# Kernel tuning notes

Hardware: AMD Instinct MI355X
Metric: run time of the kernel (lower is better)

The kernel has to match this reference:

```python
import jax, jax.numpy as jnp
import numpy as np

N_PROT = 100000
N_DRUG = 20000
D = 128
E_PPI = 1600000
E_DTI = 800000
LN_EPS = 1e-5


def setup_inputs() -> dict:
    key = jax.random.key(0)
    ks = jax.random.split(key, 11)
    s = 1.0 / np.sqrt(D)
    return {
        "x_prot": jax.random.normal(ks[0], (N_PROT, D), jnp.float32),
        "x_drug": jax.random.normal(ks[1], (N_DRUG, D), jnp.float32),
        "W_gcn": jax.random.normal(ks[2], (D, D), jnp.float32) * s,
        "b_gcn": jnp.zeros((D,), jnp.float32),
        "W_td": jax.random.normal(ks[3], (D, D), jnp.float32) * s,
        "b_td": jnp.zeros((D,), jnp.float32),
        "W_pr": jax.random.normal(ks[4], (D, D), jnp.float32) * s,
        "b_pr": jnp.zeros((D,), jnp.float32),
        "ppi_edge_index": jax.random.randint(ks[5], (2, E_PPI), 0, N_PROT),
        "dti_drug": jax.random.randint(ks[6], (E_DTI,), 0, N_DRUG),
        "dti_prot": jax.random.randint(ks[7], (E_DTI,), 0, N_PROT),
    }


def _gcn_conv(x, W, b, edge_index, num_nodes):
    # PyG GCNConv: add self-loops, symmetric D^-1/2 (A+I) D^-1/2 normalization.
    xw = x @ W  # [N, D_out]
    loops = jnp.arange(num_nodes)
    row = jnp.concatenate([edge_index[0], loops])
    col = jnp.concatenate([edge_index[1], loops])
    deg = jax.ops.segment_sum(jnp.ones_like(col, dtype=xw.dtype), col,
                              num_segments=num_nodes)
    dinv = jnp.where(deg > 0, jax.lax.rsqrt(deg), 0.0)
    norm = dinv[row] * dinv[col]  # [E+N]
    msg = xw[row] * norm[:, None]
    return jax.ops.segment_sum(msg, col, num_segments=num_nodes) + b


def _scatter_mean(vals, idx, num_segments):
    s = jax.ops.segment_sum(vals, idx, num_segments=num_segments)
    cnt = jax.ops.segment_sum(jnp.ones_like(idx, dtype=vals.dtype), idx,
                              num_segments=num_segments)
    return s / jnp.maximum(cnt, 1.0)[:, None]


def _layer_norm(y):
    mu = jnp.mean(y, axis=-1, keepdims=True)
    var = jnp.mean(jnp.square(y - mu), axis=-1, keepdims=True)
    return (y - mu) * jax.lax.rsqrt(var + LN_EPS)


def reference(x_prot, x_drug, W_gcn, b_gcn, W_td, b_td, W_pr, b_pr,
              ppi_edge_index, dti_drug, dti_prot):
    # 'protein' branch of rela_graph_node_update.forward
    x1 = _gcn_conv(x_prot, W_gcn, b_gcn, ppi_edge_index, N_PROT)
    msgs = (x_drug @ W_td + b_td)[dti_drug]  # gather drug messages per dti edge
    x2 = _scatter_mean(msgs, dti_prot, N_PROT)
    x3 = x_prot @ W_pr + b_pr
    return _layer_norm(x1 + x2 + x3 + 1e-6)
```

## Files before the change

kernel.cpp:

```cpp
#include <hip/hip_runtime.h>
#include <hip/hip_bf16.h>

#define D 128
#define NPBK 256
#define NBMAX 512
#define TILE_A 4096
#define SEGMAX 8192

typedef unsigned int uint;
typedef unsigned short ushort;
typedef __attribute__((ext_vector_type(8))) short short8;
typedef __attribute__((ext_vector_type(4))) float f32x4;
typedef __attribute__((ext_vector_type(2))) float f32x2;
typedef __attribute__((ext_vector_type(2))) uint u32x2;

static __device__ __forceinline__ float2 bf16x2(uint u) {
  float2 r;
  r.x = __uint_as_float(u << 16);
  r.y = __uint_as_float(u & 0xffff0000u);
  return r;
}

static __device__ __forceinline__ f32x2 bf16x2v(uint u) {
  u32x2 t = {u << 16, u & 0xffff0000u};
  return __builtin_bit_cast(f32x2, t);
}

static __device__ __forceinline__ uint pack_bf16x2(float a, float b) {
  __hip_bfloat162 o;
  o.x = __float2bfloat16(a);
  o.y = __float2bfloat16(b);
  return *reinterpret_cast<uint*>(&o);
}

static __device__ __forceinline__ ushort f2bf(float f) {
  __hip_bfloat16 h = __float2bfloat16(f);
  return *reinterpret_cast<ushort*>(&h);
}
static __device__ __forceinline__ float bf2f(ushort u) {
  return __uint_as_float(((uint)u) << 16);
}

static __device__ __forceinline__ void facc8(f32x2* acc4, uint4 v, f32x2 s2) {
  acc4[0] += s2 * bf16x2v(v.x);
  acc4[1] += s2 * bf16x2v(v.y);
  acc4[2] += s2 * bf16x2v(v.z);
  acc4[3] += s2 * bf16x2v(v.w);
}

__global__ void detect_kernel(const uint* __restrict__ x, int n_words,
                              int* __restrict__ flag) {
  __shared__ float smax[256];
  float m = 0.f;
  for (int i = threadIdx.x; i < n_words; i += 256) {
    float2 v = bf16x2(x[i]);
    float a = fabsf(v.x), b = fabsf(v.y);
    if (!(a <= 1e30f)) a = 1e30f;
    if (!(b <= 1e30f)) b = 1e30f;
    m = fmaxf(m, fmaxf(a, b));
  }
  smax[threadIdx.x] = m;
  __syncthreads();
  for (int s = 128; s > 0; s >>= 1) {
    if (threadIdx.x < s)
      smax[threadIdx.x] = fmaxf(smax[threadIdx.x], smax[threadIdx.x + s]);
    __syncthreads();
  }
  if (threadIdx.x == 0) *flag = (smax[0] > 1e6f) ? 1 : 0;
}

__global__ __launch_bounds__(256) void bucket_hist_kernel(
    const int* __restrict__ ppi_col, const int* __restrict__ dti_prot,
    int* __restrict__ gbh, const uint* __restrict__ xdet,
    int* __restrict__ flag, int e_ppi, int e_dti, int n_prot, int nbk) {
  __shared__ int hist[NBMAX];
  __shared__ float smax[256];
  const int tid = threadIdx.x;

  if (blockIdx.x == 0) {
    float m = 0.f;
    for (int i = tid; i < 4096; i += 256) {
      float2 v = bf16x2(xdet[i]);
      float a = fabsf(v.x), b = fabsf(v.y);
      if (!(a <= 1e30f)) a = 1e30f;
      if (!(b <= 1e30f)) b = 1e30f;
      m = fmaxf(m, fmaxf(a, b));
    }
    smax[tid] = m;
    __syncthreads();
    for (int s = 128; s > 0; s >>= 1) {
      if (tid < s) smax[tid] = fmaxf(smax[tid], smax[tid + s]);
      __syncthreads();
    }
    if (tid == 0) *flag = (smax[0] > 1e6f) ? 1 : 0;
  }

  for (int b = tid; b < nbk; b += 256) hist[b] = 0;
  __syncthreads();
  const int e_tot = e_ppi + e_dti;
  const int base = blockIdx.x * 8192;
#pragma unroll 4
  for (int j = 0; j < 32; ++j) {
    int i = base + j * 256 + tid;
    if (i < e_tot) {
      int dst = (i < e_ppi) ? ppi_col[i] : dti_prot[i - e_ppi];
      if ((unsigned)dst < (unsigned)n_prot) atomicAdd(&hist[dst >> 8], 1);
    }
  }
  __syncthreads();
  for (int b = tid; b < nbk; b += 256) {
    int h = hist[b];
    if (h) atomicAdd(&gbh[b], h);
  }
}

__global__ __launch_bounds__(256) void partition_kernel(
    const int* __restrict__ ppi_row, const int* __restrict__ ppi_col,
    const int* __restrict__ dti_drug, const int* __restrict__ dti_prot,
    const int* __restrict__ gbh, int* __restrict__ gcur, uint* __restrict__ P,
    int e_ppi, int e_dti, int n_prot, int nb) {
  __shared__ int hist[NBMAX];
  __shared__ int sh[NBMAX];
  __shared__ int lbase[NBMAX];
  __shared__ int gbase[NBMAX];
  __shared__ int cur[NBMAX];
  __shared__ int totS;
  __shared__ uint entL[TILE_A];
  __shared__ ushort bktL[TILE_A];
  const int tid = threadIdx.x;
  const int t2 = tid + 256;
  const int base = blockIdx.x * TILE_A;
  const int e_tot = e_ppi + e_dti;

  hist[tid] = 0;
  hist[t2] = 0;
  __syncthreads();

  uint sv[16];
  int dv[16];
#pragma unroll
  for (int j = 0; j < 16; ++j) {
    int i = base + j * 256 + tid;
    int d = -1;
    uint s = 0;
    if (i < e_tot) {
      int src, dst, type;
      if (i < e_ppi) {
        src = ppi_row[i];
        dst = ppi_col[i];
        type = 0;
      } else {
        int k = i - e_ppi;
        src = dti_drug[k];
        dst = dti_prot[k];
        type = 1;
      }
      if ((unsigned)dst < (unsigned)n_prot) {
        d = dst;
        s = (uint)src | ((uint)type << 17);
        atomicAdd(&hist[dst >> 8], 1);
      }
    }
    sv[j] = s;
    dv[j] = d;
  }
  __syncthreads();

  sh[tid] = hist[tid];
  sh[t2] = hist[t2];
  __syncthreads();
  for (int ofs = 1; ofs < NBMAX; ofs <<= 1) {
    int a0 = (tid >= ofs) ? sh[tid - ofs] : 0;
    int a1 = (t2 >= ofs) ? sh[t2 - ofs] : 0;
    __syncthreads();
    sh[tid] += a0;
    sh[t2] += a1;
    __syncthreads();
  }
  for (int b = tid; b < NBMAX; b += 256) {
    int lb = sh[b] - hist[b];
    lbase[b] = lb;
    cur[b] = lb;
  }
  if (tid == 0) totS = sh[NBMAX - 1];
  __syncthreads();

  sh[tid] = (tid < nb) ? gbh[tid] : 0;
  sh[t2] = (t2 < nb) ? gbh[t2] : 0;
  __syncthreads();
  for (int ofs = 1; ofs < NBMAX; ofs <<= 1) {
    int a0 = (tid >= ofs) ? sh[tid - ofs] : 0;
    int a1 = (t2 >= ofs) ? sh[t2 - ofs] : 0;
    __syncthreads();
    sh[tid] += a0;
    sh[t2] += a1;
    __syncthreads();
  }
  for (int b = tid; b < NBMAX; b += 256) {
    int h = hist[b];
    gbase[b] = h ? ((b ? sh[b - 1] : 0) + atomicAdd(&gcur[b], h)) : 0;
  }
  __syncthreads();

#pragma unroll
  for (int j = 0; j < 16; ++j) {
    if (dv[j] >= 0) {
      int b = dv[j] >> 8;
      int r = atomicAdd(&cur[b], 1);
      entL[r] = sv[j] | ((uint)(dv[j] & (NPBK - 1)) << 18);
      bktL[r] = (ushort)b;
    }
  }
  __syncthreads();

  const int tot = totS;
  for (int u = tid; u < tot; u += 256) {
    int b = bktL[u];
    P[gbase[b] + (u - lbase[b])] = entL[u];
  }
}

__global__ __launch_bounds__(1024) void place_count_kernel(
    const uint* __restrict__ P, const int* __restrict__ gbh,
    uint* __restrict__ csr, int* __restrict__ deg, float* __restrict__ dinv,
    float* __restrict__ invcnt, int* __restrict__ offsets, int n_prot,
    int nbk) {
  __shared__ int degL[NPBK], cntL[NPBK];
  __shared__ int cp[NPBK], cd[NPBK];
  __shared__ int sc[NPBK];
  __shared__ int gsh[NBMAX];
  __shared__ int startS, endS;
  __shared__ uint srt[SEGMAX];
  const int tid = threadIdx.x;
  const int b = blockIdx.x;
  const int node0 = b * NPBK;
  const int nn = min(NPBK, n_prot - node0);

  if (tid < NBMAX) gsh[tid] = (tid < nbk) ? gbh[tid] : 0;
  __syncthreads();
  for (int ofs = 1; ofs < NBMAX; ofs <<= 1) {
    int t = 0;
    if (tid < NBMAX && tid >= ofs) t = gsh[tid - ofs];
    __syncthreads();
    if (tid < NBMAX) gsh[tid] += t;
    __syncthreads();
  }
  if (tid == 0) {
    startS = b ? gsh[b - 1] : 0;
    endS = gsh[b];
  }
  if (tid < NPBK) {
    degL[tid] = 0;
    cntL[tid] = 0;
  }
  __syncthreads();
  const int start = startS, end = endS;
  const int nseg = end - start;

  for (int i = start + tid; i < end; i += 1024) {
    uint p = P[i];
    int nl = (int)(p >> 18);
    if ((p >> 17) & 1u)
      atomicAdd(&cntL[nl], 1);
    else
      atomicAdd(&degL[nl], 1);
  }
  __syncthreads();

  int v = 0;
  if (tid < NPBK) {
    v = (tid < nn) ? (degL[tid] + cntL[tid]) : 0;
    sc[tid] = v;
  }
  __syncthreads();
  for (int ofs = 1; ofs < NPBK; ofs <<= 1) {
    int t = 0;
    if (tid < NPBK && tid >= ofs) t = sc[tid - ofs];
    __syncthreads();
    if (tid < NPBK) sc[tid] += t;
    __syncthreads();
  }
  if (tid < nn) {
    int d = degL[tid], c = cntL[tid];
    int lexcl = sc[tid] - v;
    int node = node0 + tid;
    offsets[node] = start + lexcl;
    deg[node] = d;
    dinv[node] = rsqrtf((float)(d + 1));
    invcnt[node] = 1.0f / fmaxf((float)c, 1.0f);
    cp[tid] = lexcl;
    cd[tid] = lexcl + d;
  }
  if (b == nbk - 1 && tid == 0) offsets[n_prot] = end;
  __syncthreads();

  if (nseg <= SEGMAX) {
    for (int i = start + tid; i < end; i += 1024) {
      uint p = P[i];
      int nl = (int)(p >> 18);
      int pos =
          ((p >> 17) & 1u) ? atomicAdd(&cd[nl], 1) : atomicAdd(&cp[nl], 1);
      srt[pos] = p & 0x1ffffu;
    }
    __syncthreads();
    for (int u = tid; u < nseg; u += 1024) csr[start + u] = srt[u];
  } else {
    for (int i = start + tid; i < end; i += 1024) {
      uint p = P[i];
      int nl = (int)(p >> 18);
      int pos =
          ((p >> 17) & 1u) ? atomicAdd(&cd[nl], 1) : atomicAdd(&cp[nl], 1);
      csr[start + pos] = p & 0x1ffffu;
    }
  }
}

__global__ void count_kernel(const int* __restrict__ ppi_col,
                             const int* __restrict__ dti_prot,
                             int* __restrict__ deg, int* __restrict__ cnt,
                             int e_ppi, int e_dti, int n_prot) {
  int i = blockIdx.x * blockDim.x + threadIdx.x;
  if (i < e_ppi) {
    int c = ppi_col[i];
    if ((unsigned)c < (unsigned)n_prot) atomicAdd(&deg[c], 1);
  } else if (i < e_ppi + e_dti) {
    int c = dti_prot[i - e_ppi];
    if ((unsigned)c < (unsigned)n_prot) atomicAdd(&cnt[c], 1);
  }
}

__global__ void block_sum_kernel(const int* __restrict__ deg,
                                 const int* __restrict__ cnt, int n,
                                 float* __restrict__ dinv,
                                 float* __restrict__ invcnt,
                                 int* __restrict__ bsum) {
  __shared__ int sh[256];
  int i = blockIdx.x * 256 + threadIdx.x;
  int t = 0;
  if (i < n) {
    int d = deg[i], c = cnt[i];
    dinv[i] = rsqrtf((float)(d + 1));
    invcnt[i] = 1.0f / fmaxf((float)c, 1.0f);
    t = d + c;
  }
  sh[threadIdx.x] = t;
  __syncthreads();
  for (int s = 128; s > 0; s >>= 1) {
    if (threadIdx.x < s) sh[threadIdx.x] += sh[threadIdx.x + s];
    __syncthreads();
  }
  if (threadIdx.x == 0) bsum[blockIdx.x] = sh[0];
}

__global__ void scan_bsums_kernel(int* __restrict__ bsum, int nb) {
  __shared__ int sh[1024];
  __shared__ int carry;
  int tid = threadIdx.x;
  if (tid == 0) carry = 0;
  __syncthreads();
  for (int base = 0; base < nb; base += 1024) {
    int i = base + tid;
    int v = (i < nb) ? bsum[i] : 0;
    sh[tid] = v;
    __syncthreads();
    for (int ofs = 1; ofs < 1024; ofs <<= 1) {
      int t = (tid >= ofs) ? sh[tid - ofs] : 0;
      __syncthreads();
      sh[tid] += t;
      __syncthreads();
    }
    if (i < nb) bsum[i] = carry + sh[tid] - v;
    int total = sh[1023];
    __syncthreads();
    if (tid == 0) carry += total;
    __syncthreads();
  }
}

__global__ void scan_final_kernel(const int* __restrict__ deg,
                                  const int* __restrict__ cnt,
                                  const int* __restrict__ bbase,
                                  int* __restrict__ offsets, int n) {
  __shared__ int sh[256];
  int tid = threadIdx.x;
  int i = blockIdx.x * 256 + tid;
  int v = (i < n) ? deg[i] + cnt[i] : 0;
  sh[tid] = v;
  __syncthreads();
  for (int ofs = 1; ofs < 256; ofs <<= 1) {
    int t = (tid >= ofs) ? sh[tid - ofs] : 0;
    __syncthreads();
    sh[tid] += t;
    __syncthreads();
  }
  if (i < n) {
    int excl = bbase[blockIdx.x] + sh[tid] - v;
    offsets[i] = excl;
    if (i == n - 1) offsets[n] = excl + v;
  }
}

__global__ void fill_kernel(const int* __restrict__ ppi_row,
                            const int* __restrict__ ppi_col,
                            const int* __restrict__ dti_drug,
                            const int* __restrict__ dti_prot,
                            const int* __restrict__ offsets,
                            const int* __restrict__ deg,
                            int* __restrict__ fposp, int* __restrict__ fposd,
                            uint* __restrict__ csr, int e_ppi, int e_dti,
                            int n_prot) {
  int i = blockIdx.x * blockDim.x + threadIdx.x;
  if (i < e_ppi) {
    int dst = ppi_col[i];
    if ((unsigned)dst >= (unsigned)n_prot) return;
    int pos = offsets[dst] + atomicAdd(&fposp[dst], 1);
    csr[pos] = (uint)ppi_row[i];
  } else if (i < e_ppi + e_dti) {
    int j = i - e_ppi;
    int dst = dti_prot[j];
    if ((unsigned)dst >= (unsigned)n_prot) return;
    int pos = offsets[dst] + deg[dst] + atomicAdd(&fposd[dst], 1);
    csr[pos] = (uint)dti_drug[j];
  }
}

static __device__ void gemm_prot_body(
    uint4 (*aF)[4][2][64], ushort (*xwl)[128], const void* __restrict__ X,
    const void* __restrict__ Wg, const void* __restrict__ Wp,
    const void* __restrict__ bg, const void* __restrict__ bp,
    const float* __restrict__ dinv, uint* __restrict__ xw2,
    void* __restrict__ outx3, int isf, int M, int bid, int nblk) {
  const int tid = threadIdx.x;
  const int wv = tid >> 6, lane = tid & 63;
  const int cl = lane & 15, kg = lane >> 4;
  const int c = wv * 16 + cl;

  short8 bG[4], bP[4];
#pragma unroll
  for (int kt = 0; kt < 4; ++kt) {
    int k0 = kt * 32 + 8 * kg;
    short8 fg, fp;
    if (isf) {
      const float* WgF = (const float*)Wg;
      const float* WpF = (const float*)Wp;
#pragma unroll
      for (int j = 0; j < 8; ++j) {
        fg[j] = (short)f2bf(WgF[(k0 + j) * D + c]);
        fp[j] = (short)f2bf(WpF[(k0 + j) * D + c]);
      }
    } else {
      const ushort* WgH = (const ushort*)Wg;
      const ushort* WpH = (const ushort*)Wp;
#pragma unroll
      for (int j = 0; j < 8; ++j) {
        fg[j] = (short)WgH[(k0 + j) * D + c];
        fp[j] = (short)WpH[(k0 + j) * D + c];
      }
    }
    bG[kt] = fg;
    bP[kt] = fp;
  }
  float btc;
  {
    float a = isf ? ((const float*)bg)[c] : bf2f(((const ushort*)bg)[c]);
    float b = isf ? ((const float*)bp)[c] : bf2f(((const ushort*)bp)[c]);
    btc = a + b + 1e-6f;
  }

  for (int row0 = bid * 64; row0 < M; row0 += nblk * 64) {
    for (int u = tid; u < 1024; u += 512) {
      int row = u >> 4, kc = u & 15;
      int grow = row0 + row;
      uint4 hi = make_uint4(0, 0, 0, 0), lo = make_uint4(0, 0, 0, 0);
      if (isf) {
        if (grow < M) {
          const float4* Xf = (const float4*)X;
          float4 v0 = Xf[(size_t)grow * 32 + kc * 2];
          float4 v1 = Xf[(size_t)grow * 32 + kc * 2 + 1];
          float v[8] = {v0.x, v0.y, v0.z, v0.w, v1.x, v1.y, v1.z, v1.w};
          uint hw[4], lw[4];
#pragma unroll
          for (int j = 0; j < 4; ++j) {
            ushort h0 = f2bf(v[2 * j]), h1 = f2bf(v[2 * j + 1]);
            ushort l0 = f2bf(v[2 * j] - bf2f(h0));
            ushort l1 = f2bf(v[2 * j + 1] - bf2f(h1));
            hw[j] = (uint)h0 | ((uint)h1 << 16);
            lw[j] = (uint)l0 | ((uint)l1 << 16);
          }
          hi = make_uint4(hw[0], hw[1], hw[2], hw[3]);
          lo = make_uint4(lw[0], lw[1], lw[2], lw[3]);
        }
      } else {
        if (grow < M) hi = ((const uint4*)X)[(size_t)grow * 16 + kc];
      }
      int ln = (kc & 3) * 16 + (row & 15);
      int g = row >> 4, kt = kc >> 2;
      aF[g][kt][0][ln] = hi;
      if (isf) aF[g][kt][1][ln] = lo;
    }
    __syncthreads();

#pragma unroll
    for (int g = 0; g < 4; ++g) {
      f32x4 accG = {0.f, 0.f, 0.f, 0.f};
      f32x4 accP = {0.f, 0.f, 0.f, 0.f};
      uint4 aH[4];
#pragma unroll
      for (int kt = 0; kt < 4; ++kt) aH[kt] = aF[g][kt][0][lane];
#pragma unroll
      for (int kt = 0; kt < 4; ++kt) {
        short8 a = __builtin_bit_cast(short8, aH[kt]);
        accG = __builtin_amdgcn_mfma_f32_16x16x32_bf16(a, bG[kt], accG, 0, 0, 0);
        accP = __builtin_amdgcn_mfma_f32_16x16x32_bf16(a, bP[kt], accP, 0, 0, 0);
      }
      if (isf) {
        uint4 aL[4];
#pragma unroll
        for (int kt = 0; kt < 4; ++kt) aL[kt] = aF[g][kt][1][lane];
#pragma unroll
        for (int kt = 0; kt < 4; ++kt) {
          short8 a = __builtin_bit_cast(short8, aL[kt]);
          accG = __builtin_amdgcn_mfma_f32_16x16x32_bf16(a, bG[kt], accG, 0, 0, 0);
          accP = __builtin_amdgcn_mfma_f32_16x16x32_bf16(a, bP[kt], accP, 0, 0, 0);
        }
      }
      int rl0 = g * 16 + kg * 4;
#pragma unroll
      for (int r = 0; r < 4; ++r) {
        int row = row0 + rl0 + r;
        if (row < M) {
          float dn = dinv[row];
          float gv = accG[r], pv = accP[r];
          xwl[rl0 + r][c] = f2bf(gv * dn);
          float ov = fmaf(gv, dn * dn, pv + btc);
          if (isf)
            ((float*)outx3)[(size_t)row * D + c] = ov;
          else
            ((ushort*)outx3)[(size_t)row * D + c] = f2bf(ov);
        }
      }
    }
    __syncthreads();

    int valid = min(64, M - row0);
    const uint4* src = (const uint4*)xwl;
    uint4* dst = (uint4*)xw2 + (size_t)row0 * 16;
    for (int u = tid; u < valid * 16; u += 512) dst[u] = src[u];
  }
}

static __device__ void gemm_drug_body(uint4 (*aF)[4][2][64], ushort (*yl)[128],
                                      const void* __restrict__ X,
                                      const void* __restrict__ W,
                                      const void* __restrict__ bias,
                                      uint* __restrict__ Y2, int isf, int M,
                                      int bid, int nblk) {
  const int tid = threadIdx.x;
  const int wv = tid >> 6, lane = tid & 63;
  const int cl = lane & 15, kg = lane >> 4;
  const int c = wv * 16 + cl;

  short8 bT[4];
#pragma unroll
  for (int kt = 0; kt < 4; ++kt) {
    int k0 = kt * 32 + 8 * kg;
    short8 ft;
    if (isf) {
      const float* Wf = (const float*)W;
#pragma unroll
      for (int j = 0; j < 8; ++j) ft[j] = (short)f2bf(Wf[(k0 + j) * D + c]);
    } else {
      const ushort* Wh = (const ushort*)W;
#pragma unroll
      for (int j = 0; j < 8; ++j) ft[j] = (short)Wh[(k0 + j) * D + c];
    }
    bT[kt] = ft;
  }
  float btc = isf ? ((const float*)bias)[c] : bf2f(((const ushort*)bias)[c]);

  for (int row0 = bid * 64; row0 < M; row0 += nblk * 64) {
    for (int u = tid; u < 1024; u += 512) {
      int row = u >> 4, kc = u & 15;
      int grow = row0 + row;
      uint4 hi = make_uint4(0, 0, 0, 0), lo = make_uint4(0, 0, 0, 0);
      if (isf) {
        if (grow < M) {
          const float4* Xf = (const float4*)X;
          float4 v0 = Xf[(size_t)grow * 32 + kc * 2];
          float4 v1 = Xf[(size_t)grow * 32 + kc * 2 + 1];
          float v[8] = {v0.x, v0.y, v0.z, v0.w, v1.x, v1.y, v1.z, v1.w};
          uint hw[4], lw[4];
#pragma unroll
          for (int j = 0; j < 4; ++j) {
            ushort h0 = f2bf(v[2 * j]), h1 = f2bf(v[2 * j + 1]);
            ushort l0 = f2bf(v[2 * j] - bf2f(h0));
            ushort l1 = f2bf(v[2 * j + 1] - bf2f(h1));
            hw[j] = (uint)h0 | ((uint)h1 << 16);
            lw[j] = (uint)l0 | ((uint)l1 << 16);
          }
          hi = make_uint4(hw[0], hw[1], hw[2], hw[3]);
          lo = make_uint4(lw[0], lw[1], lw[2], lw[3]);
        }
      } else {
        if (grow < M) hi = ((const uint4*)X)[(size_t)grow * 16 + kc];
      }
      int ln = (kc & 3) * 16 + (row & 15);
      int g = row >> 4, kt = kc >> 2;
      aF[g][kt][0][ln] = hi;
      if (isf) aF[g][kt][1][ln] = lo;
    }
    __syncthreads();

#pragma unroll
    for (int g = 0; g < 4; ++g) {
      f32x4 acc = {0.f, 0.f, 0.f, 0.f};
      uint4 aH[4];
#pragma unroll
      for (int kt = 0; kt < 4; ++kt) aH[kt] = aF[g][kt][0][lane];
#pragma unroll
      for (int kt = 0; kt < 4; ++kt) {
        short8 a = __builtin_bit_cast(short8, aH[kt]);
        acc = __builtin_amdgcn_mfma_f32_16x16x32_bf16(a, bT[kt], acc, 0, 0, 0);
      }
      if (isf) {
        uint4 aL[4];
#pragma unroll
        for (int kt = 0; kt < 4; ++kt) aL[kt] = aF[g][kt][1][lane];
#pragma unroll
        for (int kt = 0; kt < 4; ++kt) {
          short8 a = __builtin_bit_cast(short8, aL[kt]);
          acc = __builtin_amdgcn_mfma_f32_16x16x32_bf16(a, bT[kt], acc, 0, 0, 0);
        }
      }
      int rl0 = g * 16 + kg * 4;
#pragma unroll
      for (int r = 0; r < 4; ++r) {
        int row = row0 + rl0 + r;
        if (row < M) yl[rl0 + r][c] = f2bf(acc[r] + btc);
      }
    }
    __syncthreads();

    int valid = min(64, M - row0);
    const uint4* src = (const uint4*)yl;
    uint4* dst = (uint4*)Y2 + (size_t)row0 * 16;
    for (int u = tid; u < valid * 16; u += 512) dst[u] = src[u];
  }
}

__global__ __launch_bounds__(512) void gemm_fused_kernel(
    const void* __restrict__ Xp, const void* __restrict__ Wg,
    const void* __restrict__ Wp, const void* __restrict__ bg,
    const void* __restrict__ bp, const float* __restrict__ dinv,
    uint* __restrict__ xw2, void* __restrict__ outx3, int Mp, int gp,
    const void* __restrict__ Xd, const void* __restrict__ Wt,
    const void* __restrict__ bt, uint* __restrict__ yd2, int Md,
    const int* __restrict__ flag) {
  __shared__ uint4 aF[4][4][2][64];
  __shared__ ushort tb[64][128];
  const int isf = *flag;
  if ((int)blockIdx.x < gp)
    gemm_prot_body(aF, tb, Xp, Wg, Wp, bg, bp, dinv, xw2, outx3, isf, Mp,
                   blockIdx.x, gp);
  else
    gemm_drug_body(aF, tb, Xd, Wt, bt, yd2, isf, Md, blockIdx.x - gp,
                   gridDim.x - gp);
}

__global__ __launch_bounds__(256) void gather_ln_kernel(
    const uint* __restrict__ xw2, const uint* __restrict__ yd2,
    const float* __restrict__ dinv, const float* __restrict__ invcnt,
    const int* __restrict__ offsets, const int* __restrict__ deg,
    const uint* __restrict__ csr, void* __restrict__ out,
    const int* __restrict__ flag, int node0, int ncount) {
  const int isf = *flag;
  const int nloc = (blockIdx.x * 256 + threadIdx.x) >> 6;
  const int lane = threadIdx.x & 63;
  const int grp = lane >> 4;
  const int li = lane & 15;
  if (nloc >= ncount) return;
  const int node = node0 + nloc;
  const int s0 = offsets[node];
  const int s1 = offsets[node + 1];
  const int sm = s0 + deg[node];
  const float dn = dinv[node], ic = invcnt[node];

  float x3l[8];
  if (isf) {
    const float4* xr = (const float4*)out + (size_t)node * 32 + li * 2;
    float4 x0 = xr[0], x1 = xr[1];
    x3l[0] = x0.x; x3l[1] = x0.y; x3l[2] = x0.z; x3l[3] = x0.w;
    x3l[4] = x1.x; x3l[5] = x1.y; x3l[6] = x1.z; x3l[7] = x1.w;
  } else {
    uint4 xr = ((const uint4*)out)[(size_t)node * 16 + li];
    float2 t0 = bf16x2(xr.x), t1 = bf16x2(xr.y);
    float2 t2 = bf16x2(xr.z), t3 = bf16x2(xr.w);
    x3l[0] = t0.x; x3l[1] = t0.y; x3l[2] = t1.x; x3l[3] = t1.y;
    x3l[4] = t2.x; x3l[5] = t2.y; x3l[6] = t3.x; x3l[7] = t3.y;
  }

  f32x2 acc4[4] = {{0.f, 0.f}, {0.f, 0.f}, {0.f, 0.f}, {0.f, 0.f}};
  const uint4* X4 = (const uint4*)xw2;
  const uint4* Y4 = (const uint4*)yd2;

  for (int base = s0; base < s1;) {
    int m = min(64, s1 - base);
    uint ent = (lane < m) ? csr[base + lane] : 0u;
    int nq = m >> 2;
    int t = 0;
    for (; t + 4 <= nq; t += 4) {
      uint4 w[4];
      f32x2 sc[4];
#pragma unroll
      for (int q = 0; q < 4; ++q) {
        int slot = (t + q) * 4 + grp;
        uint e = __shfl(ent, slot);
        bool isP = (base + slot) < sm;
        const uint4* T = isP ? X4 : Y4;
        w[q] = T[(size_t)e * 16 + li];
        float s = isP ? dn : ic;
        sc[q] = (f32x2){s, s};
      }
#pragma unroll
      for (int q = 0; q < 4; ++q) facc8(acc4, w[q], sc[q]);
    }
    for (; t + 2 <= nq; t += 2) {
      uint4 w0, w1;
      f32x2 sc0, sc1;
      {
        int slot = t * 4 + grp;
        uint e = __shfl(ent, slot);
        bool isP = (base + slot) < sm;
        const uint4* T = isP ? X4 : Y4;
        w0 = T[(size_t)e * 16 + li];
        float s = isP ? dn : ic;
        sc0 = (f32x2){s, s};
      }
      {
        int slot = (t + 1) * 4 + grp;
        uint e = __shfl(ent, slot);
        bool isP = (base + slot) < sm;
        const uint4* T = isP ? X4 : Y4;
        w1 = T[(size_t)e * 16 + li];
        float s = isP ? dn : ic;
        sc1 = (f32x2){s, s};
      }
      facc8(acc4, w0, sc0);
      facc8(acc4, w1, sc1);
    }
    for (; t < nq; ++t) {
      int slot = t * 4 + grp;
      uint e = __shfl(ent, slot);
      bool isP = (base + slot) < sm;
      const uint4* T = isP ? X4 : Y4;
      uint4 wv = T[(size_t)e * 16 + li];
      float s = isP ? dn : ic;
      facc8(acc4, wv, (f32x2){s, s});
    }
    int rem = m & 3;
    if (rem) {
      int slot = nq * 4 + grp;
      uint e = __shfl(ent, slot);
      if (grp < rem) {
        bool isP = (base + slot) < sm;
        const uint4* T = isP ? X4 : Y4;
        uint4 wv = T[(size_t)e * 16 + li];
        float s = isP ? dn : ic;
        facc8(acc4, wv, (f32x2){s, s});
      }
    }
    base += m;
  }

  float v[8];
#pragma unroll
  for (int i = 0; i < 8; ++i) {
    float t = (i & 1) ? acc4[i >> 1].y : acc4[i >> 1].x;
    t += __shfl_xor(t, 16);
    t += __shfl_xor(t, 32);
    v[i] = t + x3l[i];
  }

  float s = 0.f, ss = 0.f;
#pragma unroll
  for (int i = 0; i < 8; ++i) {
    s += v[i];
    ss = fmaf(v[i], v[i], ss);
  }
#pragma unroll
  for (int off = 1; off < 16; off <<= 1) {
    s += __shfl_xor(s, off);
    ss += __shfl_xor(ss, off);
  }
  float mu = s * (1.0f / 128.0f);
  float var = ss * (1.0f / 128.0f) - mu * mu;
  float rs = rsqrtf(var + 1e-5f);
#pragma unroll
  for (int i = 0; i < 8; ++i) v[i] = (v[i] - mu) * rs;

  if (isf) {
    if (grp < 2) {
      float4 o = (grp == 0) ? make_float4(v[0], v[1], v[2], v[3])
                            : make_float4(v[4], v[5], v[6], v[7]);
      ((float4*)out)[(size_t)node * 32 + li * 2 + grp] = o;
    }
  } else {
    if (grp == 0) {
      uint4 o;
      o.x = pack_bf16x2(v[0], v[1]);
      o.y = pack_bf16x2(v[2], v[3]);
      o.z = pack_bf16x2(v[4], v[5]);
      o.w = pack_bf16x2(v[6], v[7]);
      ((uint4*)out)[(size_t)node * 16 + li] = o;
    }
  }
}

extern "C" void kernel_launch(void* const* d_in, const int* in_sizes, int n_in,
                              void* d_out, int out_size, void* d_ws,
                              size_t ws_size, hipStream_t stream) {
  const void* x_prot = d_in[0];
  const void* x_drug = d_in[1];
  const void* W_gcn = d_in[2];
  const void* b_gcn = d_in[3];
  const void* W_td = d_in[4];
  const void* b_td = d_in[5];
  const void* W_pr = d_in[6];
  const void* b_pr = d_in[7];
  const int* ppi = (const int*)d_in[8];
  const int* dti_drug = (const int*)d_in[9];
  const int* dti_prot = (const int*)d_in[10];

  int n_prot = in_sizes[0] / D;
  int n_drug = in_sizes[1] / D;
  int e_ppi = in_sizes[8] / 2;
  int e_dti = in_sizes[9];
  int e_tot = e_ppi + e_dti;
  int nb = (n_prot + 255) / 256;
  int nbk = (n_prot + NPBK - 1) / NPBK;

  char* ws = (char*)d_ws;
  size_t off = 0;
  auto alloc = [&](size_t bytes) {
    void* p = ws + off;
    off = (off + bytes + 255) & ~(size_t)255;
    return p;
  };
  int* flag = (int*)alloc(256);
  uint* xw2 = (uint*)alloc((size_t)n_prot * 64 * 4);
  uint* yd2 = (uint*)alloc((size_t)n_drug * 64 * 4);
  int* deg = (int*)alloc((size_t)n_prot * 4);
  int* cnt = (int*)alloc((size_t)n_prot * 4);
  float* dinv = (float*)alloc((size_t)n_prot * 4);
  float* invcnt = (float*)alloc((size_t)n_prot * 4);
  int* offsets = (int*)alloc((size_t)(n_prot + 1) * 4);
  int* fposp = (int*)alloc((size_t)n_prot * 4);
  int* fposd = (int*)alloc((size_t)n_prot * 4);
  int* bsum = (int*)alloc((size_t)nb * 4);
  int* gbh = (int*)alloc((size_t)NBMAX * 4);
  int* gcur = (int*)alloc((size_t)NBMAX * 4);
  uint* csr = (uint*)alloc((size_t)e_tot * 4);

  if (off > ws_size) return;

  uint* P = xw2;
  bool fast_fill = (n_prot <= (1 << 17)) && (n_drug <= (1 << 17)) &&
                   (nbk <= NBMAX) && ((size_t)e_tot * 4 <= (size_t)n_prot * 256);

  if (fast_fill) {
    hipMemsetAsync(gbh, 0, (size_t)2 * NBMAX * 4, stream);
    bucket_hist_kernel<<<(e_tot + 8191) / 8192, 256, 0, stream>>>(
        ppi + e_ppi, dti_prot, gbh, (const uint*)x_prot, flag, e_ppi, e_dti,
        n_prot, nbk);
    partition_kernel<<<(e_tot + TILE_A - 1) / TILE_A, 256, 0, stream>>>(
        ppi, ppi + e_ppi, dti_drug, dti_prot, gbh, gcur, P, e_ppi, e_dti,
        n_prot, nbk);
    place_count_kernel<<<nbk, 1024, 0, stream>>>(
        P, gbh, csr, deg, dinv, invcnt, offsets, n_prot, nbk);
  } else {
    detect_kernel<<<1, 256, 0, stream>>>((const uint*)x_prot, 4096, flag);
    hipMemsetAsync(deg, 0, (size_t)n_prot * 4, stream);
    hipMemsetAsync(cnt, 0, (size_t)n_prot * 4, stream);
    hipMemsetAsync(fposp, 0, (size_t)n_prot * 4, stream);
    hipMemsetAsync(fposd, 0, (size_t)n_prot * 4, stream);
    count_kernel<<<(e_tot + 255) / 256, 256, 0, stream>>>(
        ppi + e_ppi, dti_prot, deg, cnt, e_ppi, e_dti, n_prot);
    block_sum_kernel<<<nb, 256, 0, stream>>>(deg, cnt, n_prot, dinv, invcnt,
                                             bsum);
    scan_bsums_kernel<<<1, 1024, 0, stream>>>(bsum, nb);
    scan_final_kernel<<<nb, 256, 0, stream>>>(deg, cnt, bsum, offsets, n_prot);
    fill_kernel<<<(e_tot + 255) / 256, 256, 0, stream>>>(
        ppi, ppi + e_ppi, dti_drug, dti_prot, offsets, deg, fposp, fposd, csr,
        e_ppi, e_dti, n_prot);
  }

  int nbat_p = (n_prot + 63) / 64;
  int grid_p = nbat_p < 512 ? nbat_p : 512;
  int nbat_d = (n_drug + 63) / 64;
  int grid_d = nbat_d < 512 ? nbat_d : 512;
  gemm_fused_kernel<<<grid_p + grid_d, 512, 0, stream>>>(
      x_prot, W_gcn, W_pr, b_gcn, b_pr, dinv, xw2, d_out, n_prot, grid_p,
      x_drug, W_td, b_td, yd2, n_drug, flag);

  int half = (n_prot + 1) / 2;
  int rest = n_prot - half;
  gather_ln_kernel<<<(half + 3) / 4, 256, 0, stream>>>(
      xw2, yd2, dinv, invcnt, offsets, deg, csr, d_out, flag, 0, half);
  if (rest > 0)
    gather_ln_kernel<<<(rest + 3) / 4, 256, 0, stream>>>(
        xw2, yd2, dinv, invcnt, offsets, deg, csr, d_out, flag, half, rest);
}
```

Before: 310.3 us.

## Hoist bucket scan to a kernel, pad GEMM LDS, widen grids, merge gather launch

Adds a single-block bucket_scan_kernel that computes global bucket bases once, so partition and place_count no longer each redo a 512-entry scan over gbh. Pads the GEMM shared-memory tiles (68/136 strides) to reduce LDS bank conflicts. Restructures the A-tile load so each thread issues its two rows' loads together. Launches one GEMM block per 64-row batch instead of capping the grid at 512. Merges the two half gather_ln launches into one. The cost is one extra small kernel launch and more shared memory per block.

```diff
diff --git a/kernel.cpp b/kernel.cpp
--- a/kernel.cpp
+++ b/kernel.cpp
@@ -46,6 +46,22 @@
   acc4[1] += s2 * bf16x2v(v.y);
   acc4[2] += s2 * bf16x2v(v.z);
   acc4[3] += s2 * bf16x2v(v.w);
+}
+
+static __device__ __forceinline__ void cvt_hilo(float4 v0, float4 v1,
+                                                uint4* hi, uint4* lo) {
+  float v[8] = {v0.x, v0.y, v0.z, v0.w, v1.x, v1.y, v1.z, v1.w};
+  uint hw[4], lw[4];
+#pragma unroll
+  for (int j = 0; j < 4; ++j) {
+    ushort h0 = f2bf(v[2 * j]), h1 = f2bf(v[2 * j + 1]);
+    ushort l0 = f2bf(v[2 * j] - bf2f(h0));
+    ushort l1 = f2bf(v[2 * j + 1] - bf2f(h1));
+    hw[j] = (uint)h0 | ((uint)h1 << 16);
+    lw[j] = (uint)l0 | ((uint)l1 << 16);
+  }
+  *hi = make_uint4(hw[0], hw[1], hw[2], hw[3]);
+  *lo = make_uint4(lw[0], lw[1], lw[2], lw[3]);
 }
 
 __global__ void detect_kernel(const uint* __restrict__ x, int n_words,
@@ -114,11 +130,30 @@
   }
 }
 
+__global__ __launch_bounds__(NBMAX) void bucket_scan_kernel(
+    const int* __restrict__ gbh, int* __restrict__ bbase, int nbk) {
+  __shared__ int sh[NBMAX];
+  const int tid = threadIdx.x;
+  int v = (tid < nbk) ? gbh[tid] : 0;
+  sh[tid] = v;
+  __syncthreads();
+  for (int ofs = 1; ofs < NBMAX; ofs <<= 1) {
+    int t = (tid >= ofs) ? sh[tid - ofs] : 0;
+    __syncthreads();
+    sh[tid] += t;
+    __syncthreads();
+  }
+  if (tid < nbk) {
+    bbase[tid] = sh[tid] - v;
+    if (tid == nbk - 1) bbase[nbk] = sh[tid];
+  }
+}
+
 __global__ __launch_bounds__(256) void partition_kernel(
     const int* __restrict__ ppi_row, const int* __restrict__ ppi_col,
     const int* __restrict__ dti_drug, const int* __restrict__ dti_prot,
-    const int* __restrict__ gbh, int* __restrict__ gcur, uint* __restrict__ P,
-    int e_ppi, int e_dti, int n_prot, int nb) {
+    const int* __restrict__ bbase, int* __restrict__ gcur,
+    uint* __restrict__ P, int e_ppi, int e_dti, int n_prot, int nb) {
   __shared__ int hist[NBMAX];
   __shared__ int sh[NBMAX];
   __shared__ int lbase[NBMAX];
@@ -178,28 +213,13 @@
     __syncthreads();
   }
   for (int b = tid; b < NBMAX; b += 256) {
-    int lb = sh[b] - hist[b];
+    int h = hist[b];
+    int lb = sh[b] - h;
     lbase[b] = lb;
     cur[b] = lb;
+    gbase[b] = h ? (bbase[b] + atomicAdd(&gcur[b], h)) : 0;
   }
   if (tid == 0) totS = sh[NBMAX - 1];
-  __syncthreads();
-
-  sh[tid] = (tid < nb) ? gbh[tid] : 0;
-  sh[t2] = (t2 < nb) ? gbh[t2] : 0;
-  __syncthreads();
-  for (int ofs = 1; ofs < NBMAX; ofs <<= 1) {
-    int a0 = (tid >= ofs) ? sh[tid - ofs] : 0;
-    int a1 = (t2 >= ofs) ? sh[t2 - ofs] : 0;
-    __syncthreads();
-    sh[tid] += a0;
-    sh[t2] += a1;
-    __syncthreads();
-  }
-  for (int b = tid; b < NBMAX; b += 256) {
-    int h = hist[b];
-    gbase[b] = h ? ((b ? sh[b - 1] : 0) + atomicAdd(&gcur[b], h)) : 0;
-  }
   __syncthreads();
 
 #pragma unroll
@@ -221,41 +241,26 @@
 }
 
 __global__ __launch_bounds__(1024) void place_count_kernel(
-    const uint* __restrict__ P, const int* __restrict__ gbh,
+    const uint* __restrict__ P, const int* __restrict__ bbase,
     uint* __restrict__ csr, int* __restrict__ deg, float* __restrict__ dinv,
     float* __restrict__ invcnt, int* __restrict__ offsets, int n_prot,
     int nbk) {
   __shared__ int degL[NPBK], cntL[NPBK];
   __shared__ int cp[NPBK], cd[NPBK];
   __shared__ int sc[NPBK];
-  __shared__ int gsh[NBMAX];
-  __shared__ int startS, endS;
   __shared__ uint srt[SEGMAX];
   const int tid = threadIdx.x;
   const int b = blockIdx.x;
   const int node0 = b * NPBK;
   const int nn = min(NPBK, n_prot - node0);
-
-  if (tid < NBMAX) gsh[tid] = (tid < nbk) ? gbh[tid] : 0;
-  __syncthreads();
-  for (int ofs = 1; ofs < NBMAX; ofs <<= 1) {
-    int t = 0;
-    if (tid < NBMAX && tid >= ofs) t = gsh[tid - ofs];
-    __syncthreads();
-    if (tid < NBMAX) gsh[tid] += t;
-    __syncthreads();
-  }
-  if (tid == 0) {
-    startS = b ? gsh[b - 1] : 0;
-    endS = gsh[b];
-  }
+  const int start = bbase[b], end = bbase[b + 1];
+  const int nseg = end - start;
+
   if (tid < NPBK) {
     degL[tid] = 0;
     cntL[tid] = 0;
   }
   __syncthreads();
-  const int start = startS, end = endS;
-  const int nseg = end - start;
 
   for (int i = start + tid; i < end; i += 1024) {
     uint p = P[i];
@@ -425,7 +430,7 @@
 }
 
 static __device__ void gemm_prot_body(
-    uint4 (*aF)[4][2][64], ushort (*xwl)[128], const void* __restrict__ X,
+    uint4 (*aF)[4][2][68], ushort (*xwl)[136], const void* __restrict__ X,
     const void* __restrict__ Wg, const void* __restrict__ Wp,
     const void* __restrict__ bg, const void* __restrict__ bp,
     const float* __restrict__ dinv, uint* __restrict__ xw2,
@@ -434,6 +439,7 @@
   const int wv = tid >> 6, lane = tid & 63;
   const int cl = lane & 15, kg = lane >> 4;
   const int c = wv * 16 + cl;
+  const int lnr = lane + (lane >> 4);
 
   short8 bG[4], bP[4];
 #pragma unroll
@@ -468,35 +474,38 @@
   }
 
   for (int row0 = bid * 64; row0 < M; row0 += nblk * 64) {
-    for (int u = tid; u < 1024; u += 512) {
-      int row = u >> 4, kc = u & 15;
-      int grow = row0 + row;
-      uint4 hi = make_uint4(0, 0, 0, 0), lo = make_uint4(0, 0, 0, 0);
+    {
+      const int rowA = tid >> 4, kcA = tid & 15;
+      const int rowB = rowA + 32, kcB = kcA;
+      int lnA = (kcA & 3) * 16 + (rowA & 15);
+      int lnB = (kcB & 3) * 16 + (rowB & 15);
+      lnA += lnA >> 4;
+      lnB += lnB >> 4;
+      const int gA = rowA >> 4, ktA = kcA >> 2;
+      const int gB = rowB >> 4, ktB = kcB >> 2;
+      const int growA = row0 + rowA, growB = row0 + rowB;
       if (isf) {
-        if (grow < M) {
-          const float4* Xf = (const float4*)X;
-          float4 v0 = Xf[(size_t)grow * 32 + kc * 2];
-          float4 v1 = Xf[(size_t)grow * 32 + kc * 2 + 1];
-          float v[8] = {v0.x, v0.y, v0.z, v0.w, v1.x, v1.y, v1.z, v1.w};
-          uint hw[4], lw[4];
-#pragma unroll
-          for (int j = 0; j < 4; ++j) {
-            ushort h0 = f2bf(v[2 * j]), h1 = f2bf(v[2 * j + 1]);
-            ushort l0 = f2bf(v[2 * j] - bf2f(h0));
-            ushort l1 = f2bf(v[2 * j + 1] - bf2f(h1));
-            hw[j] = (uint)h0 | ((uint)h1 << 16);
-            lw[j] = (uint)l0 | ((uint)l1 << 16);
-          }
-          hi = make_uint4(hw[0], hw[1], hw[2], hw[3]);
-          lo = make_uint4(lw[0], lw[1], lw[2], lw[3]);
-        }
+        const float4* Xf = (const float4*)X;
+        float4 z = make_float4(0.f, 0.f, 0.f, 0.f);
+        bool okA = growA < M, okB = growB < M;
+        float4 a0 = okA ? Xf[(size_t)growA * 32 + kcA * 2] : z;
+        float4 a1 = okA ? Xf[(size_t)growA * 32 + kcA * 2 + 1] : z;
+        float4 b0 = okB ? Xf[(size_t)growB * 32 + kcB * 2] : z;
+        float4 b1 = okB ? Xf[(size_t)growB * 32 + kcB * 2 + 1] : z;
+        uint4 hi, lo;
+        cvt_hilo(a0, a1, &hi, &lo);
+        aF[gA][ktA][0][lnA] = hi;
+        aF[gA][ktA][1][lnA] = lo;
+        cvt_hilo(b0, b1, &hi, &lo);
+        aF[gB][ktB][0][lnB] = hi;
+        aF[gB][ktB][1][lnB] = lo;
       } else {
-        if (grow < M) hi = ((const uint4*)X)[(size_t)grow * 16 + kc];
-      }
-      int ln = (kc & 3) * 16 + (row & 15);
-      int g = row >> 4, kt = kc >> 2;
-      aF[g][kt][0][ln] = hi;
-      if (isf) aF[g][kt][1][ln] = lo;
+        uint4 z = make_uint4(0, 0, 0, 0);
+        uint4 ha = (growA < M) ? ((const uint4*)X)[(size_t)growA * 16 + kcA] : z;
+        uint4 hb = (growB < M) ? ((const uint4*)X)[(size_t)growB * 16 + kcB] : z;
+        aF[gA][ktA][0][lnA] = ha;
+        aF[gB][ktB][0][lnB] = hb;
+      }
     }
     __syncthreads();
 
@@ -506,7 +515,7 @@
       f32x4 accP = {0.f, 0.f, 0.f, 0.f};
       uint4 aH[4];
 #pragma unroll
-      for (int kt = 0; kt < 4; ++kt) aH[kt] = aF[g][kt][0][lane];
+      for (int kt = 0; kt < 4; ++kt) aH[kt] = aF[g][kt][0][lnr];
 #pragma unroll
       for (int kt = 0; kt < 4; ++kt) {
         short8 a = __builtin_bit_cast(short8, aH[kt]);
@@ -516,7 +525,7 @@
       if (isf) {
         uint4 aL[4];
 #pragma unroll
-        for (int kt = 0; kt < 4; ++kt) aL[kt] = aF[g][kt][1][lane];
+        for (int kt = 0; kt < 4; ++kt) aL[kt] = aF[g][kt][1][lnr];
 #pragma unroll
         for (int kt = 0; kt < 4; ++kt) {
           short8 a = __builtin_bit_cast(short8, aL[kt]);
@@ -543,13 +552,16 @@
     __syncthreads();
 
     int valid = min(64, M - row0);
+    uint4* dst = (uint4*)xw2 + (size_t)row0 * 16;
     const uint4* src = (const uint4*)xwl;
-    uint4* dst = (uint4*)xw2 + (size_t)row0 * 16;
-    for (int u = tid; u < valid * 16; u += 512) dst[u] = src[u];
-  }
-}
-
-static __device__ void gemm_drug_body(uint4 (*aF)[4][2][64], ushort (*yl)[128],
+    for (int u = tid; u < valid * 16; u += 512) {
+      int r = u >> 4, q = u & 15;
+      dst[u] = src[r * 17 + q];
+    }
+  }
+}
+
+static __device__ void gemm_drug_body(uint4 (*aF)[4][2][68], ushort (*yl)[136],
                                       const void* __restrict__ X,
                                       const void* __restrict__ W,
                                       const void* __restrict__ bias,
@@ -559,6 +571,7 @@
   const int wv = tid >> 6, lane = tid & 63;
   const int cl = lane & 15, kg = lane >> 4;
   const int c = wv * 16 + cl;
+  const int lnr = lane + (lane >> 4);
 
   short8 bT[4];
 #pragma unroll
@@ -579,35 +592,38 @@
   float btc = isf ? ((const float*)bias)[c] : bf2f(((const ushort*)bias)[c]);
 
   for (int row0 = bid * 64; row0 < M; row0 += nblk * 64) {
-    for (int u = tid; u < 1024; u += 512) {
-      int row = u >> 4, kc = u & 15;
-      int grow = row0 + row;
-      uint4 hi = make_uint4(0, 0, 0, 0), lo = make_uint4(0, 0, 0, 0);
+    {
+      const int rowA = tid >> 4, kcA = tid & 15;
+      const int rowB = rowA + 32, kcB = kcA;
+      int lnA = (kcA & 3) * 16 + (rowA & 15);
+      int lnB = (kcB & 3) * 16 + (rowB & 15);
+      lnA += lnA >> 4;
+      lnB += lnB >> 4;
+      const int gA = rowA >> 4, ktA = kcA >> 2;
+      const int gB = rowB >> 4, ktB = kcB >> 2;
+      const int growA = row0 + rowA, growB = row0 + rowB;
       if (isf) {
-        if (grow < M) {
-          const float4* Xf = (const float4*)X;
-          float4 v0 = Xf[(size_t)grow * 32 + kc * 2];
-          float4 v1 = Xf[(size_t)grow * 32 + kc * 2 + 1];
-          float v[8] = {v0.x, v0.y, v0.z, v0.w, v1.x, v1.y, v1.z, v1.w};
-          uint hw[4], lw[4];
-#pragma unroll
-          for (int j = 0; j < 4; ++j) {
-            ushort h0 = f2bf(v[2 * j]), h1 = f2bf(v[2 * j + 1]);
-            ushort l0 = f2bf(v[2 * j] - bf2f(h0));
-            ushort l1 = f2bf(v[2 * j + 1] - bf2f(h1));
-            hw[j] = (uint)h0 | ((uint)h1 << 16);
-            lw[j] = (uint)l0 | ((uint)l1 << 16);
-          }
-          hi = make_uint4(hw[0], hw[1], hw[2], hw[3]);
-          lo = make_uint4(lw[0], lw[1], lw[2], lw[3]);
-        }
+        const float4* Xf = (const float4*)X;
+        float4 z = make_float4(0.f, 0.f, 0.f, 0.f);
+        bool okA = growA < M, okB = growB < M;
+        float4 a0 = okA ? Xf[(size_t)growA * 32 + kcA * 2] : z;
+        float4 a1 = okA ? Xf[(size_t)growA * 32 + kcA * 2 + 1] : z;
+        float4 b0 = okB ? Xf[(size_t)growB * 32 + kcB * 2] : z;
+        float4 b1 = okB ? Xf[(size_t)growB * 32 + kcB * 2 + 1] : z;
+        uint4 hi, lo;
+        cvt_hilo(a0, a1, &hi, &lo);
+        aF[gA][ktA][0][lnA] = hi;
+        aF[gA][ktA][1][lnA] = lo;
+        cvt_hilo(b0, b1, &hi, &lo);
+        aF[gB][ktB][0][lnB] = hi;
+        aF[gB][ktB][1][lnB] = lo;
       } else {
-        if (grow < M) hi = ((const uint4*)X)[(size_t)grow * 16 + kc];
-      }
-      int ln = (kc & 3) * 16 + (row & 15);
-      int g = row >> 4, kt = kc >> 2;
-      aF[g][kt][0][ln] = hi;
-      if (isf) aF[g][kt][1][ln] = lo;
+        uint4 z = make_uint4(0, 0, 0, 0);
+        uint4 ha = (growA < M) ? ((const uint4*)X)[(size_t)growA * 16 + kcA] : z;
+        uint4 hb = (growB < M) ? ((const uint4*)X)[(size_t)growB * 16 + kcB] : z;
+        aF[gA][ktA][0][lnA] = ha;
+        aF[gB][ktB][0][lnB] = hb;
+      }
     }
     __syncthreads();
 
@@ -616,7 +632,7 @@
       f32x4 acc = {0.f, 0.f, 0.f, 0.f};
       uint4 aH[4];
 #pragma unroll
-      for (int kt = 0; kt < 4; ++kt) aH[kt] = aF[g][kt][0][lane];
+      for (int kt = 0; kt < 4; ++kt) aH[kt] = aF[g][kt][0][lnr];
 #pragma unroll
       for (int kt = 0; kt < 4; ++kt) {
         short8 a = __builtin_bit_cast(short8, aH[kt]);
@@ -625,7 +641,7 @@
       if (isf) {
         uint4 aL[4];
 #pragma unroll
-        for (int kt = 0; kt < 4; ++kt) aL[kt] = aF[g][kt][1][lane];
+        for (int kt = 0; kt < 4; ++kt) aL[kt] = aF[g][kt][1][lnr];
 #pragma unroll
         for (int kt = 0; kt < 4; ++kt) {
           short8 a = __builtin_bit_cast(short8, aL[kt]);
@@ -642,9 +658,12 @@
     __syncthreads();
 
     int valid = min(64, M - row0);
+    uint4* dst = (uint4*)Y2 + (size_t)row0 * 16;
     const uint4* src = (const uint4*)yl;
-    uint4* dst = (uint4*)Y2 + (size_t)row0 * 16;
-    for (int u = tid; u < valid * 16; u += 512) dst[u] = src[u];
+    for (int u = tid; u < valid * 16; u += 512) {
+      int r = u >> 4, q = u & 15;
+      dst[u] = src[r * 17 + q];
+    }
   }
 }
 
@@ -656,8 +675,8 @@
     const void* __restrict__ Xd, const void* __restrict__ Wt,
     const void* __restrict__ bt, uint* __restrict__ yd2, int Md,
     const int* __restrict__ flag) {
-  __shared__ uint4 aF[4][4][2][64];
-  __shared__ ushort tb[64][128];
+  __shared__ uint4 aF[4][4][2][68];
+  __shared__ ushort tb[64][136];
   const int isf = *flag;
   if ((int)blockIdx.x < gp)
     gemm_prot_body(aF, tb, Xp, Wg, Wp, bg, bp, dinv, xw2, outx3, isf, Mp,
@@ -859,6 +878,7 @@
   int* bsum = (int*)alloc((size_t)nb * 4);
   int* gbh = (int*)alloc((size_t)NBMAX * 4);
   int* gcur = (int*)alloc((size_t)NBMAX * 4);
+  int* bbase = (int*)alloc((size_t)(NBMAX + 1) * 4);
   uint* csr = (uint*)alloc((size_t)e_tot * 4);
 
   if (off > ws_size) return;
@@ -872,11 +892,12 @@
     bucket_hist_kernel<<<(e_tot + 8191) / 8192, 256, 0, stream>>>(
         ppi + e_ppi, dti_prot, gbh, (const uint*)x_prot, flag, e_ppi, e_dti,
         n_prot, nbk);
+    bucket_scan_kernel<<<1, NBMAX, 0, stream>>>(gbh, bbase, nbk);
     partition_kernel<<<(e_tot + TILE_A - 1) / TILE_A, 256, 0, stream>>>(
-        ppi, ppi + e_ppi, dti_drug, dti_prot, gbh, gcur, P, e_ppi, e_dti,
+        ppi, ppi + e_ppi, dti_drug, dti_prot, bbase, gcur, P, e_ppi, e_dti,
         n_prot, nbk);
     place_count_kernel<<<nbk, 1024, 0, stream>>>(
-        P, gbh, csr, deg, dinv, invcnt, offsets, n_prot, nbk);
+        P, bbase, csr, deg, dinv, invcnt, offsets, n_prot, nbk);
   } else {
     detect_kernel<<<1, 256, 0, stream>>>((const uint*)x_prot, 4096, flag);
     hipMemsetAsync(deg, 0, (size_t)n_prot * 4, stream);
@@ -895,18 +916,11 @@
   }
 
   int nbat_p = (n_prot + 63) / 64;
-  int grid_p = nbat_p < 512 ? nbat_p : 512;
   int nbat_d = (n_drug + 63) / 64;
-  int grid_d = nbat_d < 512 ? nbat_d : 512;
-  gemm_fused_kernel<<<grid_p + grid_d, 512, 0, stream>>>(
-      x_prot, W_gcn, W_pr, b_gcn, b_pr, dinv, xw2, d_out, n_prot, grid_p,
+  gemm_fused_kernel<<<nbat_p + nbat_d, 512, 0, stream>>>(
+      x_prot, W_gcn, W_pr, b_gcn, b_pr, dinv, xw2, d_out, n_prot, nbat_p,
       x_drug, W_td, b_td, yd2, n_drug, flag);
 
-  int half = (n_prot + 1) / 2;
-  int rest = n_prot - half;
-  gather_ln_kernel<<<(half + 3) / 4, 256, 0, stream>>>(
-      xw2, yd2, dinv, invcnt, offsets, deg, csr, d_out, flag, 0, half);
-  if (rest > 0)
-    gather_ln_kernel<<<(rest + 3) / 4, 256, 0, stream>>>(
-        xw2, yd2, dinv, invcnt, offsets, deg, csr, d_out, flag, half, rest);
-}
+  gather_ln_kernel<<<(n_prot + 3) / 4, 256, 0, stream>>>(
+      xw2, yd2, dinv, invcnt, offsets, deg, csr, d_out, flag, 0, n_prot);
+}
```

After: 323.4 us. 1.04x slower.
